# Performance work log

Measured on AMD Instinct MI355X. Metric: run time of the kernel, lower is better.

The kernel has to match this reference:

```python
import jax, jax.numpy as jnp
import numpy as np

D_MODEL = 1024
NHEAD = 16
HEAD_DIM = D_MODEL // NHEAD
FF = 4096
ALPHA = 1.4142135  # deepnorm_alpha
WIN = (127, 128)   # sliding window (left, right)
EPS = 1e-5
ROPE_BASE = 10000.0


def rmsnorm(x, g):
    ms = jnp.mean(x * x, axis=-1, keepdims=True)
    return x * jax.lax.rsqrt(ms + EPS) * g


def rope(x):
    # x: [B, T, H, D]; non-interleaved rotary over full head dim
    T, D = x.shape[1], x.shape[-1]
    half = D // 2
    inv_freq = 1.0 / (ROPE_BASE ** (jnp.arange(half, dtype=jnp.float32) * 2.0 / D))
    ang = jnp.arange(T, dtype=jnp.float32)[:, None] * inv_freq[None, :]  # [T, half]
    cos = jnp.cos(ang)[None, :, None, :]
    sin = jnp.sin(ang)[None, :, None, :]
    x1, x2 = x[..., :half], x[..., half:]
    return jnp.concatenate([x1 * cos - x2 * sin, x2 * cos + x1 * sin], axis=-1)


def setup_inputs() -> dict:
    key = jax.random.key(0)
    ks = jax.random.split(key, 8)
    d, h = D_MODEL, FF
    return {
        "x": jax.random.normal(ks[0], (2, 2048, d), jnp.float32),
        "Wqkv": jax.random.normal(ks[1], (3 * d, d), jnp.float32) * 0.02,
        "Wout": jax.random.normal(ks[2], (d, d), jnp.float32) * 0.02,
        "bout": jnp.zeros((d,), jnp.float32),
        "W1": jax.random.normal(ks[3], (2 * h, d), jnp.float32) * 0.02,
        "W2": jax.random.normal(ks[4], (d, h), jnp.float32) * 0.02,
        "g1": jnp.ones((d,), jnp.float32),
        "g2": jnp.ones((d,), jnp.float32),
    }


def reference(x, Wqkv, Wout, bout, W1, W2, g1, g2):
    B, T, d = x.shape
    # --- self attention with RoPE + sliding window band mask ---
    qkv = (x @ Wqkv.T).reshape(B, T, 3, NHEAD, HEAD_DIM)
    q, k, v = qkv[:, :, 0], qkv[:, :, 1], qkv[:, :, 2]  # [B,T,H,Dh]
    q = rope(q)
    k = rope(k)
    q = jnp.swapaxes(q, 1, 2)  # [B,H,T,Dh]
    k = jnp.swapaxes(k, 1, 2)
    v = jnp.swapaxes(v, 1, 2)
    scale = 1.0 / np.sqrt(HEAD_DIM)
    scores = jnp.einsum('bhqd,bhkd->bhqk', q, k) * scale
    idx = jnp.arange(T)
    rel = idx[None, :] - idx[:, None]  # j - i
    band = (rel >= -WIN[0]) & (rel <= WIN[1])  # [T,T] allowed positions
    scores = jnp.where(band[None, None], scores, -jnp.inf)
    attn = jax.nn.softmax(scores, axis=-1)
    o = jnp.einsum('bhqk,bhkd->bhqd', attn, v)
    o = jnp.swapaxes(o, 1, 2).reshape(B, T, d)
    a = o @ Wout.T + bout
    # --- deepnorm residual 1 + RMSNorm ---
    x1 = a + ALPHA * x
    x2 = rmsnorm(x1, g1)
    # --- SwiGLU MLP: y, gate = fc1(x).chunk(2); y*gate*sigmoid(gate) ---
    yg = x2 @ W1.T
    y, gate = jnp.split(yg, 2, axis=-1)
    y = y * gate * jax.nn.sigmoid(gate)
    y = y @ W2.T
    # --- deepnorm residual 2 + RMSNorm ---
    x3 = y + ALPHA * x2
    return rmsnorm(x3, g2)
```

## Files before the change

### kernel.cpp

```cpp
#include <hip/hip_runtime.h>

#define T_SEQ   2048
#define NHEADS  16
#define DHEAD   64
#define DMODEL  1024
#define ALPHA_C 1.4142135f
#define EPS_C   1e-5f

typedef __attribute__((ext_vector_type(8))) short bf16x8;
typedef __attribute__((ext_vector_type(4))) short bf16x4;
typedef __attribute__((ext_vector_type(4))) float floatx4;

__device__ __forceinline__ float bf2f(unsigned short u) {
  union { unsigned int i; float f; } v;
  v.i = ((unsigned int)u) << 16;
  return v.f;
}
__device__ __forceinline__ unsigned short f2bf(float f) {
  union { float f; unsigned int i; } v;
  v.f = f;
  unsigned int u = v.i;
  u += 0x7FFF + ((u >> 16) & 1);
  return (unsigned short)(u >> 16);
}

__device__ __forceinline__ void gload_lds16(const void* g, void* l) {
  __builtin_amdgcn_global_load_lds(
      (const __attribute__((address_space(1))) void*)g,
      (__attribute__((address_space(3))) void*)l, 16, 0, 0);
}

__global__ void convert_all(const float* __restrict__ Wqkv,
                            const float* __restrict__ Wout,
                            const float* __restrict__ W1,
                            const float* __restrict__ W2,
                            const float* __restrict__ x,
                            unsigned short* __restrict__ ws)
{
  size_t i = ((size_t)blockIdx.x * 256 + threadIdx.x) * 8;
  const float* src;
  size_t off;
  if      (i <  3145728) { src = Wqkv; off = i; }
  else if (i <  4194304) { src = Wout; off = i -  3145728; }
  else if (i < 12582912) { src = W1;   off = i -  4194304; }
  else if (i < 16777216) { src = W2;   off = i - 12582912; }
  else                   { src = x;    off = i - 16777216; }
  floatx4 a = *(const floatx4*)(src + off);
  floatx4 b = *(const floatx4*)(src + off + 4);
  bf16x8 o;
  #pragma unroll
  for (int u = 0; u < 4; u++) {
    o[u]     = (short)f2bf(a[u]);
    o[4 + u] = (short)f2bf(b[u]);
  }
  *(bf16x8*)(ws + i) = o;
}

__global__ void build_rope_lut(float* __restrict__ cosT,
                               float* __restrict__ sinT)
{
  int gid = blockIdx.x * 256 + threadIdx.x;
  int t = gid >> 5, i = gid & 31;
  float fr = powf(10000.f, -(float)i * (1.f / 32.f));
  float sn, cs;
  sincosf((float)t * fr, &sn, &cs);
  cosT[gid] = cs;
  sinT[gid] = sn;
}

template<int BN>
__global__ __launch_bounds__(256) void gemm_lds(
    const unsigned short* __restrict__ A,
    const unsigned short* __restrict__ W,
    unsigned short* __restrict__ C,
    const float* __restrict__ bias,
    int M, int N, int K, int lda)
{
  constexpr int WN = BN / 2;
  constexpr int NJ = WN / 16;
  __shared__ unsigned short As[128 * 32];
  __shared__ unsigned short Bs[BN * 32];

  const int tid  = threadIdx.x;
  const int lane = tid & 63;
  const int wave = tid >> 6;
  const int wm = (wave >> 1) * 64;
  const int wn = (wave & 1) * WN;
  const int mBase = blockIdx.y * 128;
  const int nBase = blockIdx.x * BN;

  const int sRow = lane >> 2;
  const int sCol = (lane & 3) * 8;

  floatx4 acc[4][NJ];
  #pragma unroll
  for (int i = 0; i < 4; i++)
    #pragma unroll
    for (int j = 0; j < NJ; j++) acc[i][j] = (floatx4){0.f, 0.f, 0.f, 0.f};

  const int mrow = lane & 15;
  const int kq   = (lane >> 4) * 8;

  for (int kb = 0; kb < K; kb += 32) {
    __syncthreads();
    #pragma unroll
    for (int j = 0; j < 2; j++) {
      int r = wave * 32 + j * 16 + sRow;
      gload_lds16(A + (size_t)(mBase + r) * lda + kb + sCol,
                  &As[wave * 1024 + j * 512 + lane * 8]);
    }
    if constexpr (BN == 128) {
      #pragma unroll
      for (int j = 0; j < 2; j++) {
        int r = wave * 32 + j * 16 + sRow;
        gload_lds16(W + (size_t)(nBase + r) * K + kb + sCol,
                    &Bs[wave * 1024 + j * 512 + lane * 8]);
      }
    } else {
      int r = wave * 16 + sRow;
      gload_lds16(W + (size_t)(nBase + r) * K + kb + sCol,
                  &Bs[wave * 512 + lane * 8]);
    }
    __syncthreads();

    bf16x8 af[4], bfr[NJ];
    #pragma unroll
    for (int i = 0; i < 4; i++)
      af[i] = *(const bf16x8*)&As[(wm + i * 16 + mrow) * 32 + kq];
    #pragma unroll
    for (int j = 0; j < NJ; j++)
      bfr[j] = *(const bf16x8*)&Bs[(wn + j * 16 + mrow) * 32 + kq];
    #pragma unroll
    for (int i = 0; i < 4; i++)
      #pragma unroll
      for (int j = 0; j < NJ; j++)
        acc[i][j] = __builtin_amdgcn_mfma_f32_16x16x32_bf16(af[i], bfr[j], acc[i][j], 0, 0, 0);
  }

  const int col0 = lane & 15;
  const int row0 = (lane >> 4) * 4;
  #pragma unroll
  for (int j = 0; j < NJ; j++) {
    const int col = nBase + wn + j * 16 + col0;
    const float badd = bias ? bias[col] : 0.f;
    #pragma unroll
    for (int i = 0; i < 4; i++) {
      #pragma unroll
      for (int r = 0; r < 4; r++) {
        const int row = mBase + wm + i * 16 + row0 + r;
        C[(size_t)row * N + col] = f2bf(acc[i][j][r] + badd);
      }
    }
  }
}

__global__ __launch_bounds__(256) void gemm_w2_splitk(
    const unsigned short* __restrict__ A,
    const unsigned short* __restrict__ W,
    float* __restrict__ Cp)
{
  __shared__ unsigned short As[128 * 32];
  __shared__ unsigned short Bs[64 * 32];

  const int tid  = threadIdx.x;
  const int lane = tid & 63;
  const int wave = tid >> 6;
  const int wm = (wave >> 1) * 64;
  const int wn = (wave & 1) * 32;
  const int mBase = blockIdx.y * 128;
  const int nBase = blockIdx.x * 64;
  const int kOff  = blockIdx.z * 2048;

  const int sRow = lane >> 2;
  const int sCol = (lane & 3) * 8;

  floatx4 acc[4][2];
  #pragma unroll
  for (int i = 0; i < 4; i++)
    #pragma unroll
    for (int j = 0; j < 2; j++) acc[i][j] = (floatx4){0.f, 0.f, 0.f, 0.f};

  const int mrow = lane & 15;
  const int kq   = (lane >> 4) * 8;

  for (int kb = 0; kb < 2048; kb += 32) {
    __syncthreads();
    #pragma unroll
    for (int j = 0; j < 2; j++) {
      int r = wave * 32 + j * 16 + sRow;
      gload_lds16(A + (size_t)(mBase + r) * 4096 + kOff + kb + sCol,
                  &As[wave * 1024 + j * 512 + lane * 8]);
    }
    {
      int r = wave * 16 + sRow;
      gload_lds16(W + (size_t)(nBase + r) * 4096 + kOff + kb + sCol,
                  &Bs[wave * 512 + lane * 8]);
    }
    __syncthreads();

    bf16x8 af[4], bfr[2];
    #pragma unroll
    for (int i = 0; i < 4; i++)
      af[i] = *(const bf16x8*)&As[(wm + i * 16 + mrow) * 32 + kq];
    #pragma unroll
    for (int j = 0; j < 2; j++)
      bfr[j] = *(const bf16x8*)&Bs[(wn + j * 16 + mrow) * 32 + kq];
    #pragma unroll
    for (int i = 0; i < 4; i++)
      #pragma unroll
      for (int j = 0; j < 2; j++)
        acc[i][j] = __builtin_amdgcn_mfma_f32_16x16x32_bf16(af[i], bfr[j], acc[i][j], 0, 0, 0);
  }

  const int col0 = lane & 15;
  const int row0 = (lane >> 4) * 4;
  float* dst = Cp + (size_t)blockIdx.z * 4096 * 1024;
  #pragma unroll
  for (int j = 0; j < 2; j++) {
    const int col = nBase + wn + j * 16 + col0;
    #pragma unroll
    for (int i = 0; i < 4; i++)
      #pragma unroll
      for (int r = 0; r < 4; r++) {
        const int row = mBase + wm + i * 16 + row0 + r;
        dst[(size_t)row * 1024 + col] = acc[i][j][r];
      }
  }
}

__global__ __launch_bounds__(256) void gemm_qkv_rope(
    const unsigned short* __restrict__ A,
    const unsigned short* __restrict__ W,
    const float* __restrict__ cosT,
    const float* __restrict__ sinT,
    unsigned short* __restrict__ Qd,
    unsigned short* __restrict__ Kd,
    unsigned short* __restrict__ Vd)
{
  constexpr int K = 1024;
  __shared__ unsigned short As[128 * 32];
  __shared__ unsigned short Bs[128 * 32];

  const int tid  = threadIdx.x;
  const int lane = tid & 63;
  const int wave = tid >> 6;
  const int wm = (wave >> 1) * 64;
  const int wn = (wave & 1) * 64;
  const int mBase = blockIdx.y * 128;
  const int nBase = blockIdx.x * 128;

  const int sRow = lane >> 2;
  const int sCol = (lane & 3) * 8;

  floatx4 acc[4][4];
  #pragma unroll
  for (int i = 0; i < 4; i++)
    #pragma unroll
    for (int j = 0; j < 4; j++) acc[i][j] = (floatx4){0.f, 0.f, 0.f, 0.f};

  const int mrow = lane & 15;
  const int kq   = (lane >> 4) * 8;

  for (int kb = 0; kb < K; kb += 32) {
    __syncthreads();
    #pragma unroll
    for (int j = 0; j < 2; j++) {
      int r = wave * 32 + j * 16 + sRow;
      gload_lds16(A + (size_t)(mBase + r) * K + kb + sCol,
                  &As[wave * 1024 + j * 512 + lane * 8]);
      gload_lds16(W + (size_t)(nBase + r) * K + kb + sCol,
                  &Bs[wave * 1024 + j * 512 + lane * 8]);
    }
    __syncthreads();

    bf16x8 af[4], bfr[4];
    #pragma unroll
    for (int i = 0; i < 4; i++) {
      af[i]  = *(const bf16x8*)&As[(wm + i * 16 + mrow) * 32 + kq];
      bfr[i] = *(const bf16x8*)&Bs[(wn + i * 16 + mrow) * 32 + kq];
    }
    #pragma unroll
    for (int i = 0; i < 4; i++)
      #pragma unroll
      for (int j = 0; j < 4; j++)
        acc[i][j] = __builtin_amdgcn_mfma_f32_16x16x32_bf16(af[i], bfr[j], acc[i][j], 0, 0, 0);
  }

  const int col0 = lane & 15;
  const int row0 = (lane >> 4) * 4;
  const int colBase = nBase + wn;
  const int sect = colBase >> 10;
  const int h    = (colBase & 1023) >> 6;
  unsigned short* dst = (sect == 0) ? Qd : (sect == 1) ? Kd : Vd;

  if (sect < 2) {
    #pragma unroll
    for (int it = 0; it < 4; it++) {
      #pragma unroll
      for (int r = 0; r < 4; r++) {
        const int row = mBase + wm + it * 16 + row0 + r;
        const int b = row >> 11, t = row & 2047;
        size_t ob = ((size_t)((b * NHEADS + h) * T_SEQ + t)) * DHEAD;
        const int tb = t * 32;
        float c0 = cosT[tb + col0],      s0 = sinT[tb + col0];
        float c1 = cosT[tb + col0 + 16], s1 = sinT[tb + col0 + 16];
        float x1a = acc[it][0][r], x2a = acc[it][2][r];
        float x1b = acc[it][1][r], x2b = acc[it][3][r];
        dst[ob + col0]      = f2bf(x1a * c0 - x2a * s0);
        dst[ob + col0 + 32] = f2bf(x2a * c0 + x1a * s0);
        dst[ob + col0 + 16] = f2bf(x1b * c1 - x2b * s1);
        dst[ob + col0 + 48] = f2bf(x2b * c1 + x1b * s1);
      }
    }
  } else {
    #pragma unroll
    for (int it = 0; it < 4; it++)
      #pragma unroll
      for (int j = 0; j < 4; j++)
        #pragma unroll
        for (int r = 0; r < 4; r++) {
          const int row = mBase + wm + it * 16 + row0 + r;
          const int b = row >> 11, t = row & 2047;
          dst[((size_t)((b * NHEADS + h) * T_SEQ + t)) * DHEAD + j * 16 + col0] =
              f2bf(acc[it][j][r]);
        }
  }
}

#define BAR() __builtin_amdgcn_s_barrier()
#define SCB() __builtin_amdgcn_sched_barrier(0)

#define RD_A_S(bb, mh, s)                                                 \
  _Pragma("unroll") for (int i = 0; i < 4; i++)                           \
    af[i][s] = *(const bf16x8*)&lds[(bb) + aRd +                          \
        ((mh) * 64 + i * 16 + mrow) * 64 + (kq0 ^ ((s) << 5))];

#define RD_B_S(bb, s)                                                     \
  _Pragma("unroll") for (int n = 0; n < 4; n++)                           \
    bfr[n][s] = *(const bf16x8*)&lds[(bb) + bRd +                         \
        (bRow0 + n * 16 + mrow) * 64 + (kq0 ^ ((s) << 5))];

#define MFMA8(mh, nh, s)                                                  \
  _Pragma("unroll") for (int i = 0; i < 4; i++)                           \
  _Pragma("unroll") for (int n = 0; n < 2; n++)                           \
    acc[(mh) * 4 + i][(nh) * 2 + n] =                                     \
        __builtin_amdgcn_mfma_f32_16x16x32_bf16(                          \
            af[i][s], bfr[(nh) * 2 + n][s],                               \
            acc[(mh) * 4 + i][(nh) * 2 + n], 0, 0, 0);

__global__ __launch_bounds__(512, 2) void gemm_w1_swiglu_8ph(
    const unsigned short* __restrict__ A,
    const unsigned short* __restrict__ W1,
    unsigned short* __restrict__ ys)
{
  __shared__ unsigned short lds[65536];

  const int tid  = threadIdx.x;
  const int lane = tid & 63;
  const int wid  = tid >> 6;
  const int wr   = wid >> 2;
  const int wc   = wid & 3;
  const int mrow = lane & 15;
  const int quad = lane >> 4;
  const int kq0  = (quad ^ (mrow & 7)) * 8;

  const int bid  = blockIdx.y * 32 + blockIdx.x;
  const int c8   = bid & 7;
  const int u    = bid >> 3;
  const int mBase = ((c8 >> 2) * 8 + (u >> 3)) * 256;
  const int nBase = ((c8 &  3) * 8 + (u &  7)) * 128;

  const int r0 = tid >> 3;
  const int ce = (((tid & 7) ^ (r0 & 7)) * 8);
  const size_t aoff0 = (size_t)(mBase + r0) * 1024 + ce;
  const size_t aoff1 = aoff0 + (size_t)64 * 1024;
  auto growf = [&](int br) {
    int col = nBase + (br >> 6) * 32 + (br & 31);
    return ((br >> 5) & 1) ? 4096 + col : col;
  };
  const size_t boff00 = (size_t)growf(r0)       * 1024 + ce;
  const size_t boff01 = (size_t)growf(64 + r0)  * 1024 + ce;
  const size_t boff10 = (size_t)growf(128 + r0) * 1024 + ce;
  const size_t boff11 = (size_t)growf(192 + r0) * 1024 + ce;
  const int d0 = tid * 8;

  auto stA = [&](int buf, int h, int kt) {
    const unsigned short* g = A + (size_t)kt * 64 + (h ? (size_t)128 * 1024 : 0);
    int base = buf * 32768 + h * 8192;
    gload_lds16(g + aoff0, &lds[base + d0]);
    gload_lds16(g + aoff1, &lds[base + 4096 + d0]);
  };
  auto stB = [&](int buf, int h, int kt) {
    const unsigned short* g = W1 + (size_t)kt * 64;
    int base = buf * 32768 + 16384 + h * 8192;
    gload_lds16(g + (h ? boff10 : boff00), &lds[base + d0]);
    gload_lds16(g + (h ? boff11 : boff01), &lds[base + 4096 + d0]);
  };

  floatx4 acc[8][4];
  #pragma unroll
  for (int i = 0; i < 8; i++)
    #pragma unroll
    for (int n = 0; n < 4; n++) acc[i][n] = (floatx4){0.f, 0.f, 0.f, 0.f};
  bf16x8 af[4][2], bfr[4][2];

  const int aRd   = wr * 8192;
  const int bRd   = 16384 + (wc >> 1) * 8192;
  const int bRow0 = (wc & 1) * 64;

  stB(0, 0, 0); stA(0, 0, 0); stA(0, 1, 0); stB(0, 1, 0);
  stB(1, 0, 1); stA(1, 0, 1);
  asm volatile("s_waitcnt vmcnt(4)" ::: "memory");

  for (int t = 0; t < 16; ++t) {
    const int cur = t & 1;
    const int nxt = cur ^ 1;
    const int bb  = cur * 32768;
    const int ta  = (t + 1 < 16) ? t + 1 : 15;
    const int tb  = (t + 2 < 16) ? t + 2 : 15;

    BAR();
    stA(nxt, 1, ta);
    RD_A_S(bb, 0, 0); RD_B_S(bb, 0);
    SCB();
    RD_A_S(bb, 0, 1); RD_B_S(bb, 1);
    asm volatile("s_waitcnt lgkmcnt(8)" ::: "memory");
    SCB();
    __builtin_amdgcn_s_setprio(1);
    MFMA8(0, 0, 0);
    __builtin_amdgcn_s_setprio(0);
    asm volatile("s_waitcnt lgkmcnt(0)" ::: "memory");
    SCB();
    __builtin_amdgcn_s_setprio(1);
    MFMA8(0, 0, 1);
    __builtin_amdgcn_s_setprio(0);

    BAR();
    stB(nxt, 1, ta);
    __builtin_amdgcn_s_setprio(1);
    MFMA8(0, 1, 0); MFMA8(0, 1, 1);
    __builtin_amdgcn_s_setprio(0);

    BAR();
    stB(cur, 0, tb);
    RD_A_S(bb, 1, 0);
    SCB();
    RD_A_S(bb, 1, 1);
    asm volatile("s_waitcnt lgkmcnt(4)" ::: "memory");
    SCB();
    __builtin_amdgcn_s_setprio(1);
    MFMA8(1, 1, 0);
    __builtin_amdgcn_s_setprio(0);
    asm volatile("s_waitcnt lgkmcnt(0)" ::: "memory");
    SCB();
    __builtin_amdgcn_s_setprio(1);
    MFMA8(1, 1, 1);
    __builtin_amdgcn_s_setprio(0);

    BAR();
    stA(cur, 0, tb);
    __builtin_amdgcn_s_setprio(1);
    MFMA8(1, 0, 0); MFMA8(1, 0, 1);
    __builtin_amdgcn_s_setprio(0);
    asm volatile("s_waitcnt vmcnt(4)" ::: "memory");
  }

  const int col0 = lane & 15;
  const int row0 = (lane >> 4) * 4;
  #pragma unroll
  for (int n = 0; n < 2; n++) {
    const int col = nBase + wc * 32 + n * 16 + col0;
    #pragma unroll
    for (int i = 0; i < 8; i++) {
      const int rowb = mBase + wr * 128 + i * 16 + row0;
      #pragma unroll
      for (int r = 0; r < 4; r++) {
        float y = acc[i][n][r], g = acc[i][n + 2][r];
        float sig = 1.f / (1.f + __expf(-g));
        ys[(size_t)(rowb + r) * 4096 + col] = f2bf(y * g * sig);
      }
    }
  }
  asm volatile("s_waitcnt vmcnt(0)" ::: "memory");
}

__global__ __launch_bounds__(256) void attn_mfma(
    const unsigned short* __restrict__ Qg,
    const unsigned short* __restrict__ Kg,
    const unsigned short* __restrict__ Vg,
    unsigned short* __restrict__ Og)
{
  __shared__ unsigned short KV[23040];
  __shared__ unsigned short Qs[64 * 72];
  __shared__ unsigned short Ps[4 * 16 * 328];

  const int tid  = threadIdx.x;
  const int lane = tid & 63;
  const int wave = tid >> 6;
  const int c    = lane & 15;
  const int quad = lane >> 4;
  const int blk  = blockIdx.x;
  const int bh   = blk >> 5;
  const int qBase = (blk & 31) * 64;
  const size_t hbase = (size_t)bh * T_SEQ * DHEAD;

  for (int e = tid; e < 320 * 8; e += 256) {
    int row = e >> 3, ch = e & 7;
    int kg = qBase - 127 + row;
    int kgc = min(max(kg, 0), T_SEQ - 1);
    *(bf16x8*)&KV[row * 72 + ch * 8] =
        *(const bf16x8*)(Kg + hbase + (size_t)kgc * DHEAD + ch * 8);
  }
  for (int e = tid; e < 64 * 8; e += 256) {
    int row = e >> 3, ch = e & 7;
    *(bf16x8*)&Qs[row * 72 + ch * 8] =
        *(const bf16x8*)(Qg + hbase + (size_t)(qBase + row) * DHEAD + ch * 8);
  }
  __syncthreads();

  bf16x8 aq[2];
  #pragma unroll
  for (int hh = 0; hh < 2; hh++)
    aq[hh] = *(const bf16x8*)&Qs[(wave * 16 + c) * 72 + hh * 32 + quad * 8];

  floatx4 s[20];
  #pragma unroll
  for (int kt = 0; kt < 20; kt++) {
    bf16x8 b0 = *(const bf16x8*)&KV[(kt * 16 + c) * 72 + quad * 8];
    bf16x8 b1 = *(const bf16x8*)&KV[(kt * 16 + c) * 72 + 32 + quad * 8];
    floatx4 t = (floatx4){0.f, 0.f, 0.f, 0.f};
    t = __builtin_amdgcn_mfma_f32_16x16x32_bf16(aq[0], b0, t, 0, 0, 0);
    t = __builtin_amdgcn_mfma_f32_16x16x32_bf16(aq[1], b1, t, 0, 0, 0);
    s[kt] = t;
  }
  __syncthreads();

  for (int ch = wave; ch < 5; ch += 4) {
    int koff = ch * 64 + lane;
    int kg = qBase - 127 + koff;
    int kgc = min(max(kg, 0), T_SEQ - 1);
    const unsigned short* vrow = Vg + hbase + (size_t)kgc * DHEAD;
    #pragma unroll
    for (int dg = 0; dg < 8; dg++) {
      bf16x8 v8 = *(const bf16x8*)(vrow + dg * 8);
      #pragma unroll
      for (int j = 0; j < 8; j++)
        KV[(dg * 8 + j) * 328 + koff] = (unsigned short)v8[j];
    }
  }

  const int kLoMin = max(0, 127 - qBase);
  const int kHiMax = min(319, 2047 + 127 - qBase);
  float mx[4] = {-3e38f, -3e38f, -3e38f, -3e38f};
  #pragma unroll
  for (int kt = 0; kt < 20; kt++) {
    const int koff = kt * 16 + c;
    #pragma unroll
    for (int reg = 0; reg < 4; reg++) {
      const int qrow = wave * 16 + quad * 4 + reg;
      const int d = koff - qrow;
      bool ok = (d >= 0) && (d <= 255) && (koff >= kLoMin) && (koff <= kHiMax);
      float val = ok ? s[kt][reg] * 0.125f : -3e38f;
      s[kt][reg] = val;
      mx[reg] = fmaxf(mx[reg], val);
    }
  }
  #pragma unroll
  for (int reg = 0; reg < 4; reg++)
    #pragma unroll
    for (int m = 1; m <= 8; m <<= 1)
      mx[reg] = fmaxf(mx[reg], __shfl_xor(mx[reg], m));

  float ls[4] = {0.f, 0.f, 0.f, 0.f};
  #pragma unroll
  for (int kt = 0; kt < 20; kt++) {
    const int koff = kt * 16 + c;
    #pragma unroll
    for (int reg = 0; reg < 4; reg++) {
      float p = __expf(s[kt][reg] - mx[reg]);
      ls[reg] += p;
      Ps[wave * 5248 + (quad * 4 + reg) * 328 + koff] = f2bf(p);
    }
  }
  float inv[4];
  #pragma unroll
  for (int reg = 0; reg < 4; reg++) {
    #pragma unroll
    for (int m = 1; m <= 8; m <<= 1) ls[reg] += __shfl_xor(ls[reg], m);
    inv[reg] = 1.f / ls[reg];
  }
  __syncthreads();

  floatx4 oacc[4];
  #pragma unroll
  for (int nt = 0; nt < 4; nt++) oacc[nt] = (floatx4){0.f, 0.f, 0.f, 0.f};
  #pragma unroll
  for (int kt2 = 0; kt2 < 10; kt2++) {
    bf16x8 a = *(const bf16x8*)&Ps[wave * 5248 + c * 328 + kt2 * 32 + quad * 8];
    #pragma unroll
    for (int nt = 0; nt < 4; nt++) {
      bf16x8 bb = *(const bf16x8*)&KV[(nt * 16 + c) * 328 + kt2 * 32 + quad * 8];
      oacc[nt] = __builtin_amdgcn_mfma_f32_16x16x32_bf16(a, bb, oacc[nt], 0, 0, 0);
    }
  }

  const int b = bh >> 4, h = bh & 15;
  #pragma unroll
  for (int nt = 0; nt < 4; nt++) {
    #pragma unroll
    for (int reg = 0; reg < 4; reg++) {
      const int qg = qBase + wave * 16 + quad * 4 + reg;
      Og[((size_t)(b * T_SEQ + qg)) * DMODEL + h * DHEAD + nt * 16 + c] =
          f2bf(oacc[nt][reg] * inv[reg]);
    }
  }
}

__global__ __launch_bounds__(256) void rmsnorm_mid(
    const unsigned short* __restrict__ a,
    const float* __restrict__ x,
    const float* __restrict__ g,
    unsigned short* __restrict__ out)
{
  __shared__ float red[4];
  const int row = blockIdx.x;
  const int tid = threadIdx.x;
  const size_t base = (size_t)row * DMODEL;
  const int c = tid * 4;
  bf16x4  av = *(const bf16x4*)(a + base + c);
  floatx4 xv = *(const floatx4*)(x + base + c);
  floatx4 gv = *(const floatx4*)(g + c);
  float s[4], ss = 0.f;
  #pragma unroll
  for (int j = 0; j < 4; j++) {
    s[j] = bf2f((unsigned short)av[j]) + ALPHA_C * xv[j];
    ss += s[j] * s[j];
  }
  #pragma unroll
  for (int m = 1; m <= 32; m <<= 1) ss += __shfl_xor(ss, m);
  if ((tid & 63) == 0) red[tid >> 6] = ss;
  __syncthreads();
  float ms = (red[0] + red[1] + red[2] + red[3]) * (1.f / DMODEL);
  float scl = rsqrtf(ms + EPS_C);
  bf16x4 ov;
  #pragma unroll
  for (int j = 0; j < 4; j++) ov[j] = (short)f2bf(s[j] * scl * gv[j]);
  *(bf16x4*)(out + base + c) = ov;
}

__global__ __launch_bounds__(256) void rmsnorm_final_sk(
    const float* __restrict__ p0,
    const float* __restrict__ p1,
    const unsigned short* __restrict__ x2,
    const float* __restrict__ g,
    float* __restrict__ out)
{
  __shared__ float red[4];
  const int row = blockIdx.x;
  const int tid = threadIdx.x;
  const size_t base = (size_t)row * DMODEL;
  const int c = tid * 4;
  floatx4 a0 = *(const floatx4*)(p0 + base + c);
  floatx4 a1 = *(const floatx4*)(p1 + base + c);
  bf16x4  xv = *(const bf16x4*)(x2 + base + c);
  floatx4 gv = *(const floatx4*)(g + c);
  float s[4], ss = 0.f;
  #pragma unroll
  for (int j = 0; j < 4; j++) {
    s[j] = (a0[j] + a1[j]) + ALPHA_C * bf2f((unsigned short)xv[j]);
    ss += s[j] * s[j];
  }
  #pragma unroll
  for (int m = 1; m <= 32; m <<= 1) ss += __shfl_xor(ss, m);
  if ((tid & 63) == 0) red[tid >> 6] = ss;
  __syncthreads();
  float ms = (red[0] + red[1] + red[2] + red[3]) * (1.f / DMODEL);
  float scl = rsqrtf(ms + EPS_C);
  floatx4 ov;
  #pragma unroll
  for (int j = 0; j < 4; j++) ov[j] = s[j] * scl * gv[j];
  *(floatx4*)(out + base + c) = ov;
}

extern "C" void kernel_launch(void* const* d_in, const int* in_sizes, int n_in,
                              void* d_out, int out_size, void* d_ws, size_t ws_size,
                              hipStream_t stream) {
  (void)in_sizes; (void)n_in; (void)out_size; (void)ws_size;
  const float* x    = (const float*)d_in[0];
  const float* Wqkv = (const float*)d_in[1];
  const float* Wout = (const float*)d_in[2];
  const float* bout = (const float*)d_in[3];
  const float* W1   = (const float*)d_in[4];
  const float* W2   = (const float*)d_in[5];
  const float* g1   = (const float*)d_in[6];
  const float* g2   = (const float*)d_in[7];
  float* out = (float*)d_out;

  unsigned short* ws    = (unsigned short*)d_ws;
  unsigned short* Wqkvb = ws;
  unsigned short* Woutb = ws + 3145728;
  unsigned short* W1b   = ws + 4194304;
  unsigned short* W2b   = ws + 12582912;
  unsigned short* P1    = ws + 16777216;
  unsigned short* x2    = ws + 20971520;
  unsigned short* q     = ws + 25165824;
  unsigned short* k     = ws + 29360128;
  unsigned short* v     = ws + 33554432;
  unsigned short* o     = ws + 37748736;
  unsigned short* ys    = ws + 25165824;
  float* cosT = (float*)(ws + 37748736);
  float* sinT = cosT + 65536;
  float* p0   = (float*)(ws + 41943040);
  float* p1   = (float*)(ws + 50331648);

  build_rope_lut<<<256, 256, 0, stream>>>(cosT, sinT);
  convert_all<<<10240, 256, 0, stream>>>(Wqkv, Wout, W1, W2, x, ws);
  gemm_qkv_rope<<<dim3(24, 32), 256, 0, stream>>>(P1, Wqkvb, cosT, sinT, q, k, v);
  attn_mfma<<<32 * (T_SEQ / 64), 256, 0, stream>>>(q, k, v, o);
  gemm_lds<64><<<dim3(16, 32), 256, 0, stream>>>(o, Woutb, P1, bout, 4096, 1024, 1024, 1024);
  rmsnorm_mid<<<4096, 256, 0, stream>>>(P1, x, g1, x2);
  gemm_w1_swiglu_8ph<<<dim3(32, 16), 512, 0, stream>>>(x2, W1b, ys);
  gemm_w2_splitk<<<dim3(16, 32, 2), 256, 0, stream>>>(ys, W2b, p0);
  rmsnorm_final_sk<<<4096, 256, 0, stream>>>(p0, p1, x2, g2, out);
}
```

Baseline: 383.1 us.

## Restructure W1 GEMM into two-phase pipeline and rewrite W2 split-K GEMM

The W1 SwiGLU GEMM's main loop drops from four barrier-separated phases to two. Each phase now issues the full A or B prefetch and runs twice as many MFMAs between barriers. The simple single-buffered W2 split-K GEMM becomes a 512-thread, double-buffered, swizzled-LDS kernel with 256x128 tiles, a grid remap for locality, and global-to-LDS prefetch overlapped with MFMA. Both changes aim to cut barrier overhead and memory stalls. The cost is more registers, more LDS per block, and fewer, larger blocks in the W2 GEMM.

```diff
diff --git a/kernel.cpp b/kernel.cpp
--- a/kernel.cpp
+++ b/kernel.cpp
@@ -151,80 +151,6 @@
         C[(size_t)row * N + col] = f2bf(acc[i][j][r] + badd);
       }
     }
-  }
-}
-
-__global__ __launch_bounds__(256) void gemm_w2_splitk(
-    const unsigned short* __restrict__ A,
-    const unsigned short* __restrict__ W,
-    float* __restrict__ Cp)
-{
-  __shared__ unsigned short As[128 * 32];
-  __shared__ unsigned short Bs[64 * 32];
-
-  const int tid  = threadIdx.x;
-  const int lane = tid & 63;
-  const int wave = tid >> 6;
-  const int wm = (wave >> 1) * 64;
-  const int wn = (wave & 1) * 32;
-  const int mBase = blockIdx.y * 128;
-  const int nBase = blockIdx.x * 64;
-  const int kOff  = blockIdx.z * 2048;
-
-  const int sRow = lane >> 2;
-  const int sCol = (lane & 3) * 8;
-
-  floatx4 acc[4][2];
-  #pragma unroll
-  for (int i = 0; i < 4; i++)
-    #pragma unroll
-    for (int j = 0; j < 2; j++) acc[i][j] = (floatx4){0.f, 0.f, 0.f, 0.f};
-
-  const int mrow = lane & 15;
-  const int kq   = (lane >> 4) * 8;
-
-  for (int kb = 0; kb < 2048; kb += 32) {
-    __syncthreads();
-    #pragma unroll
-    for (int j = 0; j < 2; j++) {
-      int r = wave * 32 + j * 16 + sRow;
-      gload_lds16(A + (size_t)(mBase + r) * 4096 + kOff + kb + sCol,
-                  &As[wave * 1024 + j * 512 + lane * 8]);
-    }
-    {
-      int r = wave * 16 + sRow;
-      gload_lds16(W + (size_t)(nBase + r) * 4096 + kOff + kb + sCol,
-                  &Bs[wave * 512 + lane * 8]);
-    }
-    __syncthreads();
-
-    bf16x8 af[4], bfr[2];
-    #pragma unroll
-    for (int i = 0; i < 4; i++)
-      af[i] = *(const bf16x8*)&As[(wm + i * 16 + mrow) * 32 + kq];
-    #pragma unroll
-    for (int j = 0; j < 2; j++)
-      bfr[j] = *(const bf16x8*)&Bs[(wn + j * 16 + mrow) * 32 + kq];
-    #pragma unroll
-    for (int i = 0; i < 4; i++)
-      #pragma unroll
-      for (int j = 0; j < 2; j++)
-        acc[i][j] = __builtin_amdgcn_mfma_f32_16x16x32_bf16(af[i], bfr[j], acc[i][j], 0, 0, 0);
-  }
-
-  const int col0 = lane & 15;
-  const int row0 = (lane >> 4) * 4;
-  float* dst = Cp + (size_t)blockIdx.z * 4096 * 1024;
-  #pragma unroll
-  for (int j = 0; j < 2; j++) {
-    const int col = nBase + wn + j * 16 + col0;
-    #pragma unroll
-    for (int i = 0; i < 4; i++)
-      #pragma unroll
-      for (int r = 0; r < 4; r++) {
-        const int row = mBase + wm + i * 16 + row0 + r;
-        dst[(size_t)row * 1024 + col] = acc[i][j][r];
-      }
   }
 }
 
@@ -348,7 +274,7 @@
             af[i][s], bfr[(nh) * 2 + n][s],                               \
             acc[(mh) * 4 + i][(nh) * 2 + n], 0, 0, 0);
 
-__global__ __launch_bounds__(512, 2) void gemm_w1_swiglu_8ph(
+__global__ __launch_bounds__(512, 2) void gemm_w1_swiglu_2ph(
     const unsigned short* __restrict__ A,
     const unsigned short* __restrict__ W1,
     unsigned short* __restrict__ ys)
@@ -408,8 +334,9 @@
   const int bRd   = 16384 + (wc >> 1) * 8192;
   const int bRow0 = (wc & 1) * 64;
 
-  stB(0, 0, 0); stA(0, 0, 0); stA(0, 1, 0); stB(0, 1, 0);
-  stB(1, 0, 1); stA(1, 0, 1);
+  stB(0, 0, 0); stB(0, 1, 0);
+  stA(0, 0, 0); stA(0, 1, 0);
+  stB(1, 0, 1); stB(1, 1, 1);
   asm volatile("s_waitcnt vmcnt(4)" ::: "memory");
 
   for (int t = 0; t < 16; ++t) {
@@ -420,47 +347,35 @@
     const int tb  = (t + 2 < 16) ? t + 2 : 15;
 
     BAR();
-    stA(nxt, 1, ta);
+    stA(nxt, 0, ta); stA(nxt, 1, ta);
     RD_A_S(bb, 0, 0); RD_B_S(bb, 0);
     SCB();
     RD_A_S(bb, 0, 1); RD_B_S(bb, 1);
     asm volatile("s_waitcnt lgkmcnt(8)" ::: "memory");
     SCB();
     __builtin_amdgcn_s_setprio(1);
-    MFMA8(0, 0, 0);
+    MFMA8(0, 0, 0); MFMA8(0, 1, 0);
     __builtin_amdgcn_s_setprio(0);
     asm volatile("s_waitcnt lgkmcnt(0)" ::: "memory");
     SCB();
     __builtin_amdgcn_s_setprio(1);
-    MFMA8(0, 0, 1);
+    MFMA8(0, 0, 1); MFMA8(0, 1, 1);
     __builtin_amdgcn_s_setprio(0);
 
     BAR();
-    stB(nxt, 1, ta);
-    __builtin_amdgcn_s_setprio(1);
-    MFMA8(0, 1, 0); MFMA8(0, 1, 1);
-    __builtin_amdgcn_s_setprio(0);
-
-    BAR();
-    stB(cur, 0, tb);
+    stB(cur, 0, tb); stB(cur, 1, tb);
     RD_A_S(bb, 1, 0);
     SCB();
     RD_A_S(bb, 1, 1);
     asm volatile("s_waitcnt lgkmcnt(4)" ::: "memory");
     SCB();
     __builtin_amdgcn_s_setprio(1);
-    MFMA8(1, 1, 0);
+    MFMA8(1, 0, 0); MFMA8(1, 1, 0);
     __builtin_amdgcn_s_setprio(0);
     asm volatile("s_waitcnt lgkmcnt(0)" ::: "memory");
     SCB();
     __builtin_amdgcn_s_setprio(1);
-    MFMA8(1, 1, 1);
-    __builtin_amdgcn_s_setprio(0);
-
-    BAR();
-    stA(cur, 0, tb);
-    __builtin_amdgcn_s_setprio(1);
-    MFMA8(1, 0, 0); MFMA8(1, 0, 1);
+    MFMA8(1, 0, 1); MFMA8(1, 1, 1);
     __builtin_amdgcn_s_setprio(0);
     asm volatile("s_waitcnt vmcnt(4)" ::: "memory");
   }
@@ -479,6 +394,136 @@
         float sig = 1.f / (1.f + __expf(-g));
         ys[(size_t)(rowb + r) * 4096 + col] = f2bf(y * g * sig);
       }
+    }
+  }
+  asm volatile("s_waitcnt vmcnt(0)" ::: "memory");
+}
+
+#define W2_RD_A(bb, mh, s)                                                \
+  _Pragma("unroll") for (int i = 0; i < 2; i++)                           \
+    af[i][s] = *(const bf16x8*)&lds[(bb) +                                \
+        (wr * 64 + (mh) * 32 + i * 16 + mrow) * 64 + (kq0 ^ ((s) << 5))];
+
+#define W2_RD_B(bb, s)                                                    \
+  _Pragma("unroll") for (int n = 0; n < 4; n++)                           \
+    bfr[n][s] = *(const bf16x8*)&lds[(bb) + 16384 +                       \
+        (wc * 64 + n * 16 + mrow) * 64 + (kq0 ^ ((s) << 5))];
+
+#define W2_MFMA(mh, s)                                                    \
+  _Pragma("unroll") for (int i = 0; i < 2; i++)                           \
+  _Pragma("unroll") for (int n = 0; n < 4; n++)                           \
+    acc[(mh) * 2 + i][n] =                                                \
+        __builtin_amdgcn_mfma_f32_16x16x32_bf16(                          \
+            af[i][s], bfr[n][s], acc[(mh) * 2 + i][n], 0, 0, 0);
+
+__global__ __launch_bounds__(512, 2) void gemm_w2_2ph(
+    const unsigned short* __restrict__ A,
+    const unsigned short* __restrict__ W,
+    float* __restrict__ Cp)
+{
+  __shared__ unsigned short lds[49152];
+
+  const int tid  = threadIdx.x;
+  const int lane = tid & 63;
+  const int wid  = tid >> 6;
+  const int wr   = wid >> 1;
+  const int wc   = wid & 1;
+  const int mrow = lane & 15;
+  const int quad = lane >> 4;
+  const int kq0  = (quad ^ (mrow & 7)) * 8;
+
+  const int u  = blockIdx.x;
+  const int c8 = u & 7;
+  const int v  = u >> 3;
+  const int zP = v >> 4;
+  const int mBase = (((c8 >> 1) & 3) * 4 + ((v >> 2) & 3)) * 256;
+  const int nBase = ((c8 & 1) * 4 + (v & 3)) * 128;
+  const int kOff  = zP * 2048;
+
+  const int r0 = tid >> 3;
+  const int ce = (((tid & 7) ^ (r0 & 7)) * 8);
+  const int d0 = tid * 8;
+
+  auto stA = [&](int buf, int h, int kt) {
+    const unsigned short* g =
+        A + (size_t)(mBase + h * 128 + r0) * 4096 + kOff + kt * 64 + ce;
+    int base = buf * 24576 + h * 8192;
+    gload_lds16(g, &lds[base + d0]);
+    gload_lds16(g + (size_t)64 * 4096, &lds[base + 4096 + d0]);
+  };
+  auto stB = [&](int buf, int kt) {
+    const unsigned short* g =
+        W + (size_t)(nBase + r0) * 4096 + kOff + kt * 64 + ce;
+    int base = buf * 24576 + 16384;
+    gload_lds16(g, &lds[base + d0]);
+    gload_lds16(g + (size_t)64 * 4096, &lds[base + 4096 + d0]);
+  };
+
+  floatx4 acc[4][4];
+  #pragma unroll
+  for (int i = 0; i < 4; i++)
+    #pragma unroll
+    for (int n = 0; n < 4; n++) acc[i][n] = (floatx4){0.f, 0.f, 0.f, 0.f};
+  bf16x8 af[2][2], bfr[4][2];
+
+  stB(0, 0);
+  stA(0, 0, 0); stA(0, 1, 0);
+  stB(1, 1);
+  asm volatile("s_waitcnt vmcnt(2)" ::: "memory");
+
+  for (int t = 0; t < 32; ++t) {
+    const int cur = t & 1;
+    const int nxt = cur ^ 1;
+    const int bb  = cur * 24576;
+    const int ta  = (t + 1 < 32) ? t + 1 : 31;
+    const int tb  = (t + 2 < 32) ? t + 2 : 31;
+
+    BAR();
+    stA(nxt, 0, ta); stA(nxt, 1, ta);
+    W2_RD_A(bb, 0, 0); W2_RD_B(bb, 0);
+    SCB();
+    W2_RD_A(bb, 0, 1); W2_RD_B(bb, 1);
+    asm volatile("s_waitcnt lgkmcnt(6)" ::: "memory");
+    SCB();
+    __builtin_amdgcn_s_setprio(1);
+    W2_MFMA(0, 0);
+    __builtin_amdgcn_s_setprio(0);
+    asm volatile("s_waitcnt lgkmcnt(0)" ::: "memory");
+    SCB();
+    __builtin_amdgcn_s_setprio(1);
+    W2_MFMA(0, 1);
+    __builtin_amdgcn_s_setprio(0);
+
+    BAR();
+    stB(cur, tb);
+    W2_RD_A(bb, 1, 0);
+    SCB();
+    W2_RD_A(bb, 1, 1);
+    asm volatile("s_waitcnt lgkmcnt(2)" ::: "memory");
+    SCB();
+    __builtin_amdgcn_s_setprio(1);
+    W2_MFMA(1, 0);
+    __builtin_amdgcn_s_setprio(0);
+    asm volatile("s_waitcnt lgkmcnt(0)" ::: "memory");
+    SCB();
+    __builtin_amdgcn_s_setprio(1);
+    W2_MFMA(1, 1);
+    __builtin_amdgcn_s_setprio(0);
+    asm volatile("s_waitcnt vmcnt(2)" ::: "memory");
+  }
+
+  const int col0 = lane & 15;
+  const int row0 = (lane >> 4) * 4;
+  float* dst = Cp + (size_t)zP * 4096 * 1024;
+  #pragma unroll
+  for (int n = 0; n < 4; n++) {
+    const int col = nBase + wc * 64 + n * 16 + col0;
+    #pragma unroll
+    for (int i = 0; i < 4; i++) {
+      const int rowb = mBase + wr * 64 + i * 16 + row0;
+      #pragma unroll
+      for (int r = 0; r < 4; r++)
+        dst[(size_t)(rowb + r) * 1024 + col] = acc[i][n][r];
     }
   }
   asm volatile("s_waitcnt vmcnt(0)" ::: "memory");
@@ -711,7 +756,6 @@
   float* cosT = (float*)(ws + 37748736);
   float* sinT = cosT + 65536;
   float* p0   = (float*)(ws + 41943040);
-  float* p1   = (float*)(ws + 50331648);
 
   build_rope_lut<<<256, 256, 0, stream>>>(cosT, sinT);
   convert_all<<<10240, 256, 0, stream>>>(Wqkv, Wout, W1, W2, x, ws);
@@ -719,7 +763,7 @@
   attn_mfma<<<32 * (T_SEQ / 64), 256, 0, stream>>>(q, k, v, o);
   gemm_lds<64><<<dim3(16, 32), 256, 0, stream>>>(o, Woutb, P1, bout, 4096, 1024, 1024, 1024);
   rmsnorm_mid<<<4096, 256, 0, stream>>>(P1, x, g1, x2);
-  gemm_w1_swiglu_8ph<<<dim3(32, 16), 512, 0, stream>>>(x2, W1b, ys);
-  gemm_w2_splitk<<<dim3(16, 32, 2), 256, 0, stream>>>(ys, W2b, p0);
-  rmsnorm_final_sk<<<4096, 256, 0, stream>>>(p0, p1, x2, g2, out);
-}
+  gemm_w1_swiglu_2ph<<<dim3(32, 16), 512, 0, stream>>>(x2, W1b, ys);
+  gemm_w2_2ph<<<256, 512, 0, stream>>>(ys, W2b, p0);
+  rmsnorm_final_sk<<<4096, 256, 0, stream>>>(p0, p0 + 4194304, x2, g2, out);
+}
```

After: 359.3 us. 1.07x faster.
